# Kernel tuning notes

Hardware: AMD Instinct MI355X
Metric: run time of the kernel (lower is better)

The kernel has to match this reference:

```python
import jax, jax.numpy as jnp
import numpy as np


def _lstm_layer(x_seq, w_ih, w_hh, b_ih, b_hh):
    # x_seq: [T, in], PyTorch gate order i, f, g, o
    H = w_hh.shape[1]
    h0 = jnp.zeros((H,), x_seq.dtype)

    def step(carry, x_t):
        h, c = carry
        gates = x_t @ w_ih.T + h @ w_hh.T + b_ih + b_hh  # [4H]
        i, f, g, o = jnp.split(gates, 4)
        i = jax.nn.sigmoid(i)
        f = jax.nn.sigmoid(f)
        g = jnp.tanh(g)
        o = jax.nn.sigmoid(o)
        c = f * c + i * g
        h = o * jnp.tanh(c)
        return (h, c), h

    _, hs = jax.lax.scan(step, (h0, h0), x_seq)
    return hs  # [T, H]


def setup_inputs() -> dict:
    key = jax.random.key(0)
    ks = jax.random.split(key, 12)
    B, T, n, H = 8, 128, 32, 128
    s = 1.0 / np.sqrt(H)

    def u(k, shape):
        return jax.random.uniform(k, shape, jnp.float32, -s, s)

    return {
        "x": jax.random.normal(ks[0], (B, T, n, n), jnp.float32),
        "w_ih0": u(ks[1], (4 * H, 1)),
        "w_hh0": u(ks[2], (4 * H, H)),
        "b_ih0": u(ks[3], (4 * H,)),
        "b_hh0": u(ks[4], (4 * H,)),
        "w_ih1": u(ks[5], (4 * H, H)),
        "w_hh1": u(ks[6], (4 * H, H)),
        "b_ih1": u(ks[7], (4 * H,)),
        "b_hh1": u(ks[8], (4 * H,)),
        "w_out": u(ks[9], (1, H)),
        "b_out": u(ks[10], (1,)),
    }


def reference(x, w_ih0, w_hh0, b_ih0, b_hh0, w_ih1, w_hh1, b_ih1, b_hh1, w_out, b_out):
    # x: [B, T, n, n]
    def rnn_forward(xi):  # xi: [T, n, n] -> out [T, 1]
        u = jnp.trace(xi, axis1=-2, axis2=-1)[:, None]  # [T, 1]
        h1 = _lstm_layer(u, w_ih0, w_hh0, b_ih0, b_hh0)
        h2 = _lstm_layer(h1, w_ih1, w_hh1, b_ih1, b_hh1)
        return h2 @ w_out.T + b_out  # [T, 1]

    jac = jax.vmap(jax.jacrev(rnn_forward))(x)  # [B, T, 1, T, n, n]
    d = jnp.diagonal(jac, axis1=1, axis2=3)      # [B, 1, n, n, T]
    # mirror torch: [:, 0] then transpose(2,3).transpose(1,2) -> [B, T, n, n]
    return jnp.transpose(d[:, 0], (0, 3, 1, 2))
```

## Files before the change

kernel.cpp:

```cpp
#include <hip/hip_runtime.h>
#include <math.h>

#define H    128
#define TT   128
#define CH   8
#define NCH  (TT / CH)

#define OFF_H1V   0
#define OFF_PARTS 262144
#define OFF_CNT   1441792

__device__ __forceinline__ float sigf(float x)       { return 1.0f / (1.0f + __expf(-x)); }
__device__ __forceinline__ float tanhf_fast(float x) { return 1.0f - 2.0f / (1.0f + __expf(2.0f * x)); }

__device__ __forceinline__ float quad_sum(float v) {
    int t = __builtin_amdgcn_update_dpp(0, __float_as_int(v), 0xB1, 0xF, 0xF, true);
    v += __int_as_float(t);
    t = __builtin_amdgcn_update_dpp(0, __float_as_int(v), 0x4E, 0xF, 0xF, true);
    v += __int_as_float(t);
    return v;
}

__device__ __forceinline__ void wait_ge(int* ptr, int val) {
    while (__hip_atomic_load(ptr, __ATOMIC_RELAXED, __HIP_MEMORY_SCOPE_AGENT) < val)
        __builtin_amdgcn_s_sleep(1);
    (void)__hip_atomic_load(ptr, __ATOMIC_ACQUIRE, __HIP_MEMORY_SCOPE_AGENT);
}

#define BARRIER_LGKM() do { \
    asm volatile("s_waitcnt lgkmcnt(0)" ::: "memory"); \
    __builtin_amdgcn_s_barrier(); \
    asm volatile("" ::: "memory"); \
} while (0)

#define BARRIER_ALL() do { \
    asm volatile("s_waitcnt vmcnt(0) lgkmcnt(0)" ::: "memory"); \
    __builtin_amdgcn_s_barrier(); \
    asm volatile("" ::: "memory"); \
} while (0)

#define DECLW4(nm, src) \
    float4 _t_##nm = (src); \
    float nm##_x = _t_##nm.x, nm##_y = _t_##nm.y, nm##_z = _t_##nm.z, nm##_w = _t_##nm.w; \
    asm volatile("" : "+v"(nm##_x), "+v"(nm##_y), "+v"(nm##_z), "+v"(nm##_w));

#define LOADW_ALL(W) \
    const float4* wpa_ = (const float4*)((W) + (size_t)(rg)       * H + p * 32); \
    const float4* wpb_ = (const float4*)((W) + (size_t)(rg + 128) * H + p * 32); \
    const float4* wpc_ = (const float4*)((W) + (size_t)(rg + 256) * H + p * 32); \
    const float4* wpd_ = (const float4*)((W) + (size_t)(rg + 384) * H + p * 32); \
    DECLW4(wa0, wpa_[0]) DECLW4(wa1, wpa_[1]) DECLW4(wa2, wpa_[2]) DECLW4(wa3, wpa_[3]) \
    DECLW4(wa4, wpa_[4]) DECLW4(wa5, wpa_[5]) DECLW4(wa6, wpa_[6]) DECLW4(wa7, wpa_[7]) \
    DECLW4(wb0, wpb_[0]) DECLW4(wb1, wpb_[1]) DECLW4(wb2, wpb_[2]) DECLW4(wb3, wpb_[3]) \
    DECLW4(wb4, wpb_[4]) DECLW4(wb5, wpb_[5]) DECLW4(wb6, wpb_[6]) DECLW4(wb7, wpb_[7]) \
    DECLW4(wc0, wpc_[0]) DECLW4(wc1, wpc_[1]) DECLW4(wc2, wpc_[2]) DECLW4(wc3, wpc_[3]) \
    DECLW4(wc4, wpc_[4]) DECLW4(wc5, wpc_[5]) DECLW4(wc6, wpc_[6]) DECLW4(wc7, wpc_[7]) \
    DECLW4(wd0, wpd_[0]) DECLW4(wd1, wpd_[1]) DECLW4(wd2, wpd_[2]) DECLW4(wd3, wpd_[3]) \
    DECLW4(wd4, wpd_[4]) DECLW4(wd5, wpd_[5]) DECLW4(wd6, wpd_[6]) DECLW4(wd7, wpd_[7])

#define FMA1(nm, ov, acc) \
    acc = fmaf(nm##_x, ov.x, acc); acc = fmaf(nm##_y, ov.y, acc); \
    acc = fmaf(nm##_z, ov.z, acc); acc = fmaf(nm##_w, ov.w, acc);

#define DOTJ(j) FMA1(wa##j, hv##j, a0) FMA1(wb##j, hv##j, a1) FMA1(wc##j, hv##j, a2) FMA1(wd##j, hv##j, a3)

#define DOT_BODY(HBASE) \
    const float4* _hp4 = (const float4*)(HBASE); \
    float4 hv0=_hp4[0],hv1=_hp4[1],hv2=_hp4[2],hv3=_hp4[3], \
           hv4=_hp4[4],hv5=_hp4[5],hv6=_hp4[6],hv7=_hp4[7]; \
    float a0=0.f,a1=0.f,a2=0.f,a3=0.f; \
    DOTJ(0) DOTJ(1) DOTJ(2) DOTJ(3) DOTJ(4) DOTJ(5) DOTJ(6) DOTJ(7) \
    a0 = quad_sum(a0); a1 = quad_sum(a1); a2 = quad_sum(a2); a3 = quad_sum(a3);

__global__ __launch_bounds__(512, 1)
void pipe_kernel(const float* __restrict__ x,
                 const float* __restrict__ w_ih0,
                 const float* __restrict__ w_hh0,
                 const float* __restrict__ b_ih0,
                 const float* __restrict__ b_hh0,
                 const float* __restrict__ w_ih1,
                 const float* __restrict__ w_hh1,
                 const float* __restrict__ b_ih1,
                 const float* __restrict__ b_hh1,
                 const float* __restrict__ w_out,
                 float* __restrict__ ws,
                 float* __restrict__ outp) {
    const int role = blockIdx.x >> 3;
    const int b    = blockIdx.x & 7;
    const int r    = threadIdx.x;
    const int rg   = r >> 2, p = r & 3;
    const int wsl  = rg >> 5, wpos = rg & 31;

    int* cntA  = (int*)ws + OFF_CNT       + b * 32;
    int* cntB1 = (int*)ws + OFF_CNT + 256 + b * 32;
    int* cntB2 = (int*)ws + OFF_CNT + 512 + b * 32;
    float* h1v = ws + OFF_H1V + (size_t)b * TT * 256;

    __shared__ float hbuf[2][144];
    __shared__ float u_s[TT];
    __shared__ float scr[512];
    __shared__ float hb[CH * 144];
    __shared__ float gbuf[CH][128];

    if (role == 0) {
        LOADW_ALL(w_hh0)
        const float b0 = b_ih0[rg]       + b_hh0[rg];
        const float b1 = b_ih0[rg + 128] + b_hh0[rg + 128];
        const float b2 = b_ih0[rg + 256] + b_hh0[rg + 256];
        const float b3 = b_ih0[rg + 384] + b_hh0[rg + 384];
        const float wi0 = w_ih0[rg], wi1 = w_ih0[rg + 128];
        const float wi2 = w_ih0[rg + 256], wi3 = w_ih0[rg + 384];
        {
            const float* xb = x + (size_t)(b * TT + (r & 127)) * 1024;
            const int pq = r >> 7;
            float u = 0.f;
#pragma unroll
            for (int i = 0; i < 8; i++) u += xb[(pq * 8 + i) * 33];
            scr[r] = u;
        }
        if (r < 144) hbuf[0][r] = 0.f;
        __syncthreads();
        if (r < TT) u_s[r] = scr[r] + scr[r + 128] + scr[r + 256] + scr[r + 384];
        __syncthreads();

        float c1 = 0.f;
        float hn_prev = 0.f, vn_prev = 0.f;
        for (int t = 0; t < TT; t++) {
            if (t & (CH - 1)) {
                if (p == 0) h1v[(t - 1) * 256 + rg] = hn_prev;
                if (p == 1) h1v[(t - 1) * 256 + 128 + rg] = vn_prev;
            }
            const float u = u_s[t];
            const float* hc = hbuf[t & 1];
            float* hx = hbuf[(t & 1) ^ 1];
            DOT_BODY(hc + p * 36)
            float z0 = a0 + fmaf(wi0, u, b0);
            float z1 = a1 + fmaf(wi1, u, b1);
            float z2 = a2 + fmaf(wi2, u, b2);
            float z3 = a3 + fmaf(wi3, u, b3);
            float gi = sigf(z0), gf = sigf(z1), gg = tanhf_fast(z2), go = sigf(z3);
            float di = gi * (1.f - gi) * wi0, df = gf * (1.f - gf) * wi1;
            float dg = (1.f - gg * gg) * wi2, dd = go * (1.f - go) * wi3;
            float dc = df * c1 + di * gg + gi * dg;
            c1 = gf * c1 + gi * gg;
            float th = tanhf_fast(c1);
            float hn = go * th;
            float vn = dd * th + go * (1.f - th * th) * dc;
            if (p == wsl) hx[p * 36 + wpos] = hn;
            if ((t & (CH - 1)) == CH - 1) {
                if (p == 0) h1v[t * 256 + rg] = hn;
                if (p == 1) h1v[t * 256 + 128 + rg] = vn;
                BARRIER_ALL();
                if (r == 0)
                    __hip_atomic_store(cntA, t + 1, __ATOMIC_RELEASE, __HIP_MEMORY_SCOPE_AGENT);
            } else {
                hn_prev = hn; vn_prev = vn;
                BARRIER_LGKM();
            }
        }
    } else if (role == 1 || role == 2) {
        LOADW_ALL(w_ih1)
        int* myCnt = (role == 2) ? cntB2 : cntB1;
        const float* hsrc = h1v + ((role == 2) ? 128 : 0);
        float* pbase = ws + OFF_PARTS + (size_t)b * TT * 1024 + ((role == 2) ? 512 : 0);
        for (int c = 0; c < NCH; c++) {
            if (r == 0) wait_ge(cntA, (c + 1) * CH);
            __syncthreads();
            if (r < 256) {
                int tl = r >> 5, k4 = r & 31, s = k4 >> 3, j = k4 & 7;
                float4 v = *(const float4*)(hsrc + (size_t)(c * CH + tl) * 256 + k4 * 4);
                *(float4*)&hb[(tl * 4 + s) * 36 + j * 4] = v;
            }
            __syncthreads();
#pragma unroll
            for (int tl = 0; tl < CH; tl++) {
                DOT_BODY(hb + (tl * 4 + p) * 36)
                float sel = (p == 0) ? a0 : (p == 1) ? a1 : (p == 2) ? a2 : a3;
                pbase[(size_t)(c * CH + tl) * 1024 + r] = sel;
            }
            BARRIER_ALL();
            if (r == 0)
                __hip_atomic_store(myCnt, (c + 1) * CH, __ATOMIC_RELEASE, __HIP_MEMORY_SCOPE_AGENT);
        }
    } else {
        LOADW_ALL(w_hh1)
        const float b0 = b_ih1[rg]       + b_hh1[rg];
        const float b1 = b_ih1[rg + 128] + b_hh1[rg + 128];
        const float b2 = b_ih1[rg + 256] + b_hh1[rg + 256];
        const float b3 = b_ih1[rg + 384] + b_hh1[rg + 384];
        const float wo = w_out[rg];
        if (r < 144) hbuf[0][r] = 0.f;
        __syncthreads();
        const float* parts = ws + OFF_PARTS + (size_t)b * TT * 1024;
        float c2 = 0.f;
        for (int c = 0; c < NCH; c++) {
            if (r == 0) { wait_ge(cntB1, (c + 1) * CH); wait_ge(cntB2, (c + 1) * CH); }
            __syncthreads();
            float4 zf[CH], af[CH];
#pragma unroll
            for (int tl = 0; tl < CH; tl++) {
                zf[tl] = *(const float4*)(parts + (size_t)(c * CH + tl) * 1024 + rg * 4);
                af[tl] = *(const float4*)(parts + (size_t)(c * CH + tl) * 1024 + 512 + rg * 4);
            }
#pragma unroll
            for (int tl = 0; tl < CH; tl++) {
                const int t = c * CH + tl;
                const float* hc = hbuf[t & 1];
                float* hx = hbuf[(t & 1) ^ 1];
                DOT_BODY(hc + p * 36)
                float z0 = a0 + b0 + zf[tl].x;
                float z1 = a1 + b1 + zf[tl].y;
                float z2 = a2 + b2 + zf[tl].z;
                float z3 = a3 + b3 + zf[tl].w;
                float gi = sigf(z0), gf = sigf(z1), gg = tanhf_fast(z2), go = sigf(z3);
                float di = gi * (1.f - gi) * af[tl].x, df = gf * (1.f - gf) * af[tl].y;
                float dg = (1.f - gg * gg) * af[tl].z, dd = go * (1.f - go) * af[tl].w;
                float dc = df * c2 + di * gg + gi * dg;
                c2 = gf * c2 + gi * gg;
                float th = tanhf_fast(c2);
                if (p == wsl) hx[p * 36 + wpos] = go * th;
                float dh2 = dd * th + go * (1.f - th * th) * dc;
                if (p == 0) gbuf[tl][rg] = wo * dh2;
                BARRIER_LGKM();
            }
            {
                const int w = r >> 6, l = r & 63;
                float v = gbuf[w][l] + gbuf[w][l + 64];
                v = quad_sum(v);
                v += __shfl_xor(v, 4, 64);
                v += __shfl_xor(v, 8, 64);
                v += __shfl_xor(v, 16, 64);
                v += __shfl_xor(v, 32, 64);
                if (l == 0) scr[w] = v;
                BARRIER_LGKM();
                if (r < 256) {
                    const int tl = r >> 5, d = r & 31;
                    outp[(size_t)(b * TT + c * CH + tl) * 1024 + d * 33] = scr[tl];
                }
            }
        }
    }
}

extern "C" void kernel_launch(void* const* d_in, const int* in_sizes, int n_in,
                              void* d_out, int out_size, void* d_ws, size_t ws_size,
                              hipStream_t stream) {
    const float* x     = (const float*)d_in[0];
    const float* w_ih0 = (const float*)d_in[1];
    const float* w_hh0 = (const float*)d_in[2];
    const float* b_ih0 = (const float*)d_in[3];
    const float* b_hh0 = (const float*)d_in[4];
    const float* w_ih1 = (const float*)d_in[5];
    const float* w_hh1 = (const float*)d_in[6];
    const float* b_ih1 = (const float*)d_in[7];
    const float* b_hh1 = (const float*)d_in[8];
    const float* w_out = (const float*)d_in[9];

    float* ws = (float*)d_ws;

    hipMemsetAsync(d_out, 0, (size_t)out_size, stream);

    pipe_kernel<<<dim3(32), dim3(512), 0, stream>>>(x, w_ih0, w_hh0, b_ih0, b_hh0,
                                                    w_ih1, w_hh1, b_ih1, b_hh1, w_out,
                                                    ws, (float*)d_out);
}
```

Measured before the change: 240.3 us.

## Split LSTM recurrent dot products across 8 lanes with 1024-thread blocks

Doubles the block size to 1024 threads so each gate row's 128-wide dot product is split across 8 lanes of 16 elements instead of 4 lanes of 32. The extra cross-lane step uses a DPP row reduction, and the shared hidden-state buffers are re-laid out with a stride of 20. The aim is to shorten the serial per-timestep critical path of the recurrence and halve the per-thread weight registers. In exchange, barriers now span twice as many waves, reductions gain a step, and the layer-2 block loads its pre-activations per step instead of prefetching a whole chunk.

```diff
diff --git a/kernel.cpp b/kernel.cpp
--- a/kernel.cpp
+++ b/kernel.cpp
@@ -20,6 +20,11 @@
     v += __int_as_float(t);
     return v;
 }
+__device__ __forceinline__ float sum8(float v) {
+    v = quad_sum(v);
+    int t = __builtin_amdgcn_update_dpp(0, __float_as_int(v), 0x141, 0xF, 0xF, true);
+    return v + __int_as_float(t);
+}
 
 __device__ __forceinline__ void wait_ge(int* ptr, int val) {
     while (__hip_atomic_load(ptr, __ATOMIC_RELAXED, __HIP_MEMORY_SCOPE_AGENT) < val)
@@ -45,18 +50,14 @@
     asm volatile("" : "+v"(nm##_x), "+v"(nm##_y), "+v"(nm##_z), "+v"(nm##_w));
 
 #define LOADW_ALL(W) \
-    const float4* wpa_ = (const float4*)((W) + (size_t)(rg)       * H + p * 32); \
-    const float4* wpb_ = (const float4*)((W) + (size_t)(rg + 128) * H + p * 32); \
-    const float4* wpc_ = (const float4*)((W) + (size_t)(rg + 256) * H + p * 32); \
-    const float4* wpd_ = (const float4*)((W) + (size_t)(rg + 384) * H + p * 32); \
+    const float4* wpa_ = (const float4*)((W) + (size_t)(rg)       * H + p * 16); \
+    const float4* wpb_ = (const float4*)((W) + (size_t)(rg + 128) * H + p * 16); \
+    const float4* wpc_ = (const float4*)((W) + (size_t)(rg + 256) * H + p * 16); \
+    const float4* wpd_ = (const float4*)((W) + (size_t)(rg + 384) * H + p * 16); \
     DECLW4(wa0, wpa_[0]) DECLW4(wa1, wpa_[1]) DECLW4(wa2, wpa_[2]) DECLW4(wa3, wpa_[3]) \
-    DECLW4(wa4, wpa_[4]) DECLW4(wa5, wpa_[5]) DECLW4(wa6, wpa_[6]) DECLW4(wa7, wpa_[7]) \
     DECLW4(wb0, wpb_[0]) DECLW4(wb1, wpb_[1]) DECLW4(wb2, wpb_[2]) DECLW4(wb3, wpb_[3]) \
-    DECLW4(wb4, wpb_[4]) DECLW4(wb5, wpb_[5]) DECLW4(wb6, wpb_[6]) DECLW4(wb7, wpb_[7]) \
     DECLW4(wc0, wpc_[0]) DECLW4(wc1, wpc_[1]) DECLW4(wc2, wpc_[2]) DECLW4(wc3, wpc_[3]) \
-    DECLW4(wc4, wpc_[4]) DECLW4(wc5, wpc_[5]) DECLW4(wc6, wpc_[6]) DECLW4(wc7, wpc_[7]) \
-    DECLW4(wd0, wpd_[0]) DECLW4(wd1, wpd_[1]) DECLW4(wd2, wpd_[2]) DECLW4(wd3, wpd_[3]) \
-    DECLW4(wd4, wpd_[4]) DECLW4(wd5, wpd_[5]) DECLW4(wd6, wpd_[6]) DECLW4(wd7, wpd_[7])
+    DECLW4(wd0, wpd_[0]) DECLW4(wd1, wpd_[1]) DECLW4(wd2, wpd_[2]) DECLW4(wd3, wpd_[3])
 
 #define FMA1(nm, ov, acc) \
     acc = fmaf(nm##_x, ov.x, acc); acc = fmaf(nm##_y, ov.y, acc); \
@@ -66,13 +67,15 @@
 
 #define DOT_BODY(HBASE) \
     const float4* _hp4 = (const float4*)(HBASE); \
-    float4 hv0=_hp4[0],hv1=_hp4[1],hv2=_hp4[2],hv3=_hp4[3], \
-           hv4=_hp4[4],hv5=_hp4[5],hv6=_hp4[6],hv7=_hp4[7]; \
+    float4 hv0=_hp4[0],hv1=_hp4[1],hv2=_hp4[2],hv3=_hp4[3]; \
     float a0=0.f,a1=0.f,a2=0.f,a3=0.f; \
-    DOTJ(0) DOTJ(1) DOTJ(2) DOTJ(3) DOTJ(4) DOTJ(5) DOTJ(6) DOTJ(7) \
-    a0 = quad_sum(a0); a1 = quad_sum(a1); a2 = quad_sum(a2); a3 = quad_sum(a3);
-
-__global__ __launch_bounds__(512, 1)
+    DOTJ(0) DOTJ(1) DOTJ(2) DOTJ(3) \
+    a0 = sum8(a0); a1 = sum8(a1); a2 = sum8(a2); a3 = sum8(a3);
+
+#define SLS 20
+#define HSZ (8 * SLS)
+
+__global__ __launch_bounds__(1024, 1)
 void pipe_kernel(const float* __restrict__ x,
                  const float* __restrict__ w_ih0,
                  const float* __restrict__ w_hh0,
@@ -88,18 +91,18 @@
     const int role = blockIdx.x >> 3;
     const int b    = blockIdx.x & 7;
     const int r    = threadIdx.x;
-    const int rg   = r >> 2, p = r & 3;
-    const int wsl  = rg >> 5, wpos = rg & 31;
+    const int rg   = r >> 3, p = r & 7;
+    const int wsl  = rg >> 4, wpos = rg & 15;
 
     int* cntA  = (int*)ws + OFF_CNT       + b * 32;
     int* cntB1 = (int*)ws + OFF_CNT + 256 + b * 32;
     int* cntB2 = (int*)ws + OFF_CNT + 512 + b * 32;
     float* h1v = ws + OFF_H1V + (size_t)b * TT * 256;
 
-    __shared__ float hbuf[2][144];
+    __shared__ float hbuf[2][HSZ];
     __shared__ float u_s[TT];
-    __shared__ float scr[512];
-    __shared__ float hb[CH * 144];
+    __shared__ float scr[1024];
+    __shared__ float hb[CH * HSZ];
     __shared__ float gbuf[CH][128];
 
     if (role == 0) {
@@ -115,12 +118,17 @@
             const int pq = r >> 7;
             float u = 0.f;
 #pragma unroll
-            for (int i = 0; i < 8; i++) u += xb[(pq * 8 + i) * 33];
+            for (int i = 0; i < 4; i++) u += xb[(pq * 4 + i) * 33];
             scr[r] = u;
         }
-        if (r < 144) hbuf[0][r] = 0.f;
+        if (r < HSZ) hbuf[0][r] = 0.f;
         __syncthreads();
-        if (r < TT) u_s[r] = scr[r] + scr[r + 128] + scr[r + 256] + scr[r + 384];
+        if (r < TT) {
+            float s = 0.f;
+#pragma unroll
+            for (int k = 0; k < 8; k++) s += scr[r + 128 * k];
+            u_s[r] = s;
+        }
         __syncthreads();
 
         float c1 = 0.f;
@@ -133,7 +141,7 @@
             const float u = u_s[t];
             const float* hc = hbuf[t & 1];
             float* hx = hbuf[(t & 1) ^ 1];
-            DOT_BODY(hc + p * 36)
+            DOT_BODY(hc + p * SLS)
             float z0 = a0 + fmaf(wi0, u, b0);
             float z1 = a1 + fmaf(wi1, u, b1);
             float z2 = a2 + fmaf(wi2, u, b2);
@@ -146,7 +154,7 @@
             float th = tanhf_fast(c1);
             float hn = go * th;
             float vn = dd * th + go * (1.f - th * th) * dc;
-            if (p == wsl) hx[p * 36 + wpos] = hn;
+            if (p == wsl) hx[p * SLS + wpos] = hn;
             if ((t & (CH - 1)) == CH - 1) {
                 if (p == 0) h1v[t * 256 + rg] = hn;
                 if (p == 1) h1v[t * 256 + 128 + rg] = vn;
@@ -167,16 +175,18 @@
             if (r == 0) wait_ge(cntA, (c + 1) * CH);
             __syncthreads();
             if (r < 256) {
-                int tl = r >> 5, k4 = r & 31, s = k4 >> 3, j = k4 & 7;
+                int tl = r >> 5, k4 = r & 31;
                 float4 v = *(const float4*)(hsrc + (size_t)(c * CH + tl) * 256 + k4 * 4);
-                *(float4*)&hb[(tl * 4 + s) * 36 + j * 4] = v;
+                *(float4*)&hb[tl * HSZ + (k4 >> 2) * SLS + (k4 & 3) * 4] = v;
             }
             __syncthreads();
 #pragma unroll
             for (int tl = 0; tl < CH; tl++) {
-                DOT_BODY(hb + (tl * 4 + p) * 36)
-                float sel = (p == 0) ? a0 : (p == 1) ? a1 : (p == 2) ? a2 : a3;
-                pbase[(size_t)(c * CH + tl) * 1024 + r] = sel;
+                DOT_BODY(hb + tl * HSZ + p * SLS)
+                if (p < 4) {
+                    float sel = (p == 0) ? a0 : (p == 1) ? a1 : (p == 2) ? a2 : a3;
+                    pbase[(size_t)(c * CH + tl) * 1024 + rg * 4 + p] = sel;
+                }
             }
             BARRIER_ALL();
             if (r == 0)
@@ -189,49 +199,48 @@
         const float b2 = b_ih1[rg + 256] + b_hh1[rg + 256];
         const float b3 = b_ih1[rg + 384] + b_hh1[rg + 384];
         const float wo = w_out[rg];
-        if (r < 144) hbuf[0][r] = 0.f;
+        if (r < HSZ) hbuf[0][r] = 0.f;
         __syncthreads();
         const float* parts = ws + OFF_PARTS + (size_t)b * TT * 1024;
         float c2 = 0.f;
         for (int c = 0; c < NCH; c++) {
             if (r == 0) { wait_ge(cntB1, (c + 1) * CH); wait_ge(cntB2, (c + 1) * CH); }
             __syncthreads();
-            float4 zf[CH], af[CH];
-#pragma unroll
-            for (int tl = 0; tl < CH; tl++) {
-                zf[tl] = *(const float4*)(parts + (size_t)(c * CH + tl) * 1024 + rg * 4);
-                af[tl] = *(const float4*)(parts + (size_t)(c * CH + tl) * 1024 + 512 + rg * 4);
-            }
 #pragma unroll
             for (int tl = 0; tl < CH; tl++) {
                 const int t = c * CH + tl;
+                const float* pt = parts + (size_t)t * 1024 + rg * 4;
+                float4 zf = *(const float4*)pt;
+                float4 af = *(const float4*)(pt + 512);
                 const float* hc = hbuf[t & 1];
                 float* hx = hbuf[(t & 1) ^ 1];
-                DOT_BODY(hc + p * 36)
-                float z0 = a0 + b0 + zf[tl].x;
-                float z1 = a1 + b1 + zf[tl].y;
-                float z2 = a2 + b2 + zf[tl].z;
-                float z3 = a3 + b3 + zf[tl].w;
+                DOT_BODY(hc + p * SLS)
+                float z0 = a0 + b0 + zf.x;
+                float z1 = a1 + b1 + zf.y;
+                float z2 = a2 + b2 + zf.z;
+                float z3 = a3 + b3 + zf.w;
                 float gi = sigf(z0), gf = sigf(z1), gg = tanhf_fast(z2), go = sigf(z3);
-                float di = gi * (1.f - gi) * af[tl].x, df = gf * (1.f - gf) * af[tl].y;
-                float dg = (1.f - gg * gg) * af[tl].z, dd = go * (1.f - go) * af[tl].w;
+                float di = gi * (1.f - gi) * af.x, df = gf * (1.f - gf) * af.y;
+                float dg = (1.f - gg * gg) * af.z, dd = go * (1.f - go) * af.w;
                 float dc = df * c2 + di * gg + gi * dg;
                 c2 = gf * c2 + gi * gg;
                 float th = tanhf_fast(c2);
-                if (p == wsl) hx[p * 36 + wpos] = go * th;
+                if (p == wsl) hx[p * SLS + wpos] = go * th;
                 float dh2 = dd * th + go * (1.f - th * th) * dc;
                 if (p == 0) gbuf[tl][rg] = wo * dh2;
                 BARRIER_LGKM();
             }
             {
-                const int w = r >> 6, l = r & 63;
-                float v = gbuf[w][l] + gbuf[w][l + 64];
-                v = quad_sum(v);
-                v += __shfl_xor(v, 4, 64);
-                v += __shfl_xor(v, 8, 64);
-                v += __shfl_xor(v, 16, 64);
-                v += __shfl_xor(v, 32, 64);
-                if (l == 0) scr[w] = v;
+                if (r < 512) {
+                    const int w = r >> 6, l = r & 63;
+                    float v = gbuf[w][l] + gbuf[w][l + 64];
+                    v = quad_sum(v);
+                    v += __shfl_xor(v, 4, 64);
+                    v += __shfl_xor(v, 8, 64);
+                    v += __shfl_xor(v, 16, 64);
+                    v += __shfl_xor(v, 32, 64);
+                    if (l == 0) scr[w] = v;
+                }
                 BARRIER_LGKM();
                 if (r < 256) {
                     const int tl = r >> 5, d = r & 31;
@@ -260,7 +269,7 @@
 
     hipMemsetAsync(d_out, 0, (size_t)out_size, stream);
 
-    pipe_kernel<<<dim3(32), dim3(512), 0, stream>>>(x, w_ih0, w_hh0, b_ih0, b_hh0,
-                                                    w_ih1, w_hh1, b_ih1, b_hh1, w_out,
-                                                    ws, (float*)d_out);
-}
+    pipe_kernel<<<dim3(32), dim3(1024), 0, stream>>>(x, w_ih0, w_hh0, b_ih0, b_hh0,
+                                                     w_ih1, w_hh1, b_ih1, b_hh1, w_out,
+                                                     ws, (float*)d_out);
+}
```

Result: slower. 285.5 us (+18.8%).

## Remap thread layout and broadcast h via DPP to cut LDS reads

Applied to the files above, without the earlier changes.

Threads are remapped so each lane loads only two float4 of the hidden state from LDS instead of eight. The remaining values are broadcast across each group of four lanes with DPP quad permutes, and the cross-slice reduction uses row-shift DPP sums. The consumer role now loads its per-step partials inside the loop instead of prefetching a whole chunk into registers, and the launch bounds loosen to allow up to two waves per EU. The aim is to lower LDS bandwidth and latency on the serial recurrent critical path, at the cost of extra DPP instructions and possibly more exposed global-load latency.

```diff
diff --git a/kernel.cpp b/kernel.cpp
--- a/kernel.cpp
+++ b/kernel.cpp
@@ -13,6 +13,13 @@
 __device__ __forceinline__ float sigf(float x)       { return 1.0f / (1.0f + __expf(-x)); }
 __device__ __forceinline__ float tanhf_fast(float x) { return 1.0f - 2.0f / (1.0f + __expf(2.0f * x)); }
 
+__device__ __forceinline__ float sum4s(float v) {
+    int t = __builtin_amdgcn_update_dpp(0, __float_as_int(v), 0x124, 0xF, 0xF, true);
+    v += __int_as_float(t);
+    t = __builtin_amdgcn_update_dpp(0, __float_as_int(v), 0x128, 0xF, 0xF, true);
+    v += __int_as_float(t);
+    return v;
+}
 __device__ __forceinline__ float quad_sum(float v) {
     int t = __builtin_amdgcn_update_dpp(0, __float_as_int(v), 0xB1, 0xF, 0xF, true);
     v += __int_as_float(t);
@@ -58,21 +65,30 @@
     DECLW4(wd0, wpd_[0]) DECLW4(wd1, wpd_[1]) DECLW4(wd2, wpd_[2]) DECLW4(wd3, wpd_[3]) \
     DECLW4(wd4, wpd_[4]) DECLW4(wd5, wpd_[5]) DECLW4(wd6, wpd_[6]) DECLW4(wd7, wpd_[7])
 
-#define FMA1(nm, ov, acc) \
-    acc = fmaf(nm##_x, ov.x, acc); acc = fmaf(nm##_y, ov.y, acc); \
-    acc = fmaf(nm##_z, ov.z, acc); acc = fmaf(nm##_w, ov.w, acc);
-
-#define DOTJ(j) FMA1(wa##j, hv##j, a0) FMA1(wb##j, hv##j, a1) FMA1(wc##j, hv##j, a2) FMA1(wd##j, hv##j, a3)
-
-#define DOT_BODY(HBASE) \
-    const float4* _hp4 = (const float4*)(HBASE); \
-    float4 hv0=_hp4[0],hv1=_hp4[1],hv2=_hp4[2],hv3=_hp4[3], \
-           hv4=_hp4[4],hv5=_hp4[5],hv6=_hp4[6],hv7=_hp4[7]; \
-    float a0=0.f,a1=0.f,a2=0.f,a3=0.f; \
-    DOTJ(0) DOTJ(1) DOTJ(2) DOTJ(3) DOTJ(4) DOTJ(5) DOTJ(6) DOTJ(7) \
-    a0 = quad_sum(a0); a1 = quad_sum(a1); a2 = quad_sum(a2); a3 = quad_sum(a3);
-
-__global__ __launch_bounds__(512, 1)
+#define QB(dst, src, ctrl) \
+    dst = __int_as_float(__builtin_amdgcn_update_dpp(0, __float_as_int(src), ctrl, 0xF, 0xF, true));
+
+#define FMAQ(g, A, B, acc) \
+    acc = fmaf(g##A##_x, h0_, acc); acc = fmaf(g##A##_y, h1_, acc); \
+    acc = fmaf(g##A##_z, h2_, acc); acc = fmaf(g##A##_w, h3_, acc); \
+    acc = fmaf(g##B##_x, h4_, acc); acc = fmaf(g##B##_y, h5_, acc); \
+    acc = fmaf(g##B##_z, h6_, acc); acc = fmaf(g##B##_w, h7_, acc);
+
+#define QUARTER(A, B, ctrl) { \
+    float h0_, h1_, h2_, h3_, h4_, h5_, h6_, h7_; \
+    QB(h0_, hA_.x, ctrl) QB(h1_, hA_.y, ctrl) QB(h2_, hA_.z, ctrl) QB(h3_, hA_.w, ctrl) \
+    QB(h4_, hB_.x, ctrl) QB(h5_, hB_.y, ctrl) QB(h6_, hB_.z, ctrl) QB(h7_, hB_.w, ctrl) \
+    FMAQ(wa, A, B, a0) FMAQ(wb, A, B, a1) FMAQ(wc, A, B, a2) FMAQ(wd, A, B, a3) }
+
+#define DOT_BODY(HB) \
+    const float4* _hq = (const float4*)((HB) + p * 36 + lo * 8); \
+    float4 hA_ = _hq[0], hB_ = _hq[1]; \
+    float a0 = 0.f, a1 = 0.f, a2 = 0.f, a3 = 0.f; \
+    QUARTER(0, 1, 0x00) QUARTER(2, 3, 0x55) QUARTER(4, 5, 0xAA) QUARTER(6, 7, 0xFF) \
+    a0 = sum4s(a0); a1 = sum4s(a1); a2 = sum4s(a2); a3 = sum4s(a3);
+
+__global__ __launch_bounds__(512)
+__attribute__((amdgpu_waves_per_eu(1, 2)))
 void pipe_kernel(const float* __restrict__ x,
                  const float* __restrict__ w_ih0,
                  const float* __restrict__ w_hh0,
@@ -88,7 +104,9 @@
     const int role = blockIdx.x >> 3;
     const int b    = blockIdx.x & 7;
     const int r    = threadIdx.x;
-    const int rg   = r >> 2, p = r & 3;
+    const int p    = (r >> 2) & 3;
+    const int lo   = r & 3;
+    const int rg   = lo | ((r >> 4) << 2);
     const int wsl  = rg >> 5, wpos = rg & 31;
 
     int* cntA  = (int*)ws + OFF_CNT       + b * 32;
@@ -96,10 +114,10 @@
     int* cntB2 = (int*)ws + OFF_CNT + 512 + b * 32;
     float* h1v = ws + OFF_H1V + (size_t)b * TT * 256;
 
-    __shared__ float hbuf[2][144];
+    __shared__ __align__(16) float hbuf[2][144];
     __shared__ float u_s[TT];
     __shared__ float scr[512];
-    __shared__ float hb[CH * 144];
+    __shared__ __align__(16) float hb[CH * 144];
     __shared__ float gbuf[CH][128];
 
     if (role == 0) {
@@ -133,7 +151,7 @@
             const float u = u_s[t];
             const float* hc = hbuf[t & 1];
             float* hx = hbuf[(t & 1) ^ 1];
-            DOT_BODY(hc + p * 36)
+            DOT_BODY(hc)
             float z0 = a0 + fmaf(wi0, u, b0);
             float z1 = a1 + fmaf(wi1, u, b1);
             float z2 = a2 + fmaf(wi2, u, b2);
@@ -146,7 +164,7 @@
             float th = tanhf_fast(c1);
             float hn = go * th;
             float vn = dd * th + go * (1.f - th * th) * dc;
-            if (p == wsl) hx[p * 36 + wpos] = hn;
+            if (p == wsl) hx[wsl * 36 + wpos] = hn;
             if ((t & (CH - 1)) == CH - 1) {
                 if (p == 0) h1v[t * 256 + rg] = hn;
                 if (p == 1) h1v[t * 256 + 128 + rg] = vn;
@@ -163,6 +181,7 @@
         int* myCnt = (role == 2) ? cntB2 : cntB1;
         const float* hsrc = h1v + ((role == 2) ? 128 : 0);
         float* pbase = ws + OFF_PARTS + (size_t)b * TT * 1024 + ((role == 2) ? 512 : 0);
+        const int sidx = (rg << 2) | p;
         for (int c = 0; c < NCH; c++) {
             if (r == 0) wait_ge(cntA, (c + 1) * CH);
             __syncthreads();
@@ -174,9 +193,9 @@
             __syncthreads();
 #pragma unroll
             for (int tl = 0; tl < CH; tl++) {
-                DOT_BODY(hb + (tl * 4 + p) * 36)
+                DOT_BODY(hb + tl * 144)
                 float sel = (p == 0) ? a0 : (p == 1) ? a1 : (p == 2) ? a2 : a3;
-                pbase[(size_t)(c * CH + tl) * 1024 + r] = sel;
+                pbase[(size_t)(c * CH + tl) * 1024 + sidx] = sel;
             }
             BARRIER_ALL();
             if (r == 0)
@@ -196,29 +215,26 @@
         for (int c = 0; c < NCH; c++) {
             if (r == 0) { wait_ge(cntB1, (c + 1) * CH); wait_ge(cntB2, (c + 1) * CH); }
             __syncthreads();
-            float4 zf[CH], af[CH];
-#pragma unroll
-            for (int tl = 0; tl < CH; tl++) {
-                zf[tl] = *(const float4*)(parts + (size_t)(c * CH + tl) * 1024 + rg * 4);
-                af[tl] = *(const float4*)(parts + (size_t)(c * CH + tl) * 1024 + 512 + rg * 4);
-            }
 #pragma unroll
             for (int tl = 0; tl < CH; tl++) {
                 const int t = c * CH + tl;
+                const float* pt = parts + (size_t)t * 1024 + rg * 4;
+                float4 zf = *(const float4*)pt;
+                float4 af = *(const float4*)(pt + 512);
                 const float* hc = hbuf[t & 1];
                 float* hx = hbuf[(t & 1) ^ 1];
-                DOT_BODY(hc + p * 36)
-                float z0 = a0 + b0 + zf[tl].x;
-                float z1 = a1 + b1 + zf[tl].y;
-                float z2 = a2 + b2 + zf[tl].z;
-                float z3 = a3 + b3 + zf[tl].w;
+                DOT_BODY(hc)
+                float z0 = a0 + b0 + zf.x;
+                float z1 = a1 + b1 + zf.y;
+                float z2 = a2 + b2 + zf.z;
+                float z3 = a3 + b3 + zf.w;
                 float gi = sigf(z0), gf = sigf(z1), gg = tanhf_fast(z2), go = sigf(z3);
-                float di = gi * (1.f - gi) * af[tl].x, df = gf * (1.f - gf) * af[tl].y;
-                float dg = (1.f - gg * gg) * af[tl].z, dd = go * (1.f - go) * af[tl].w;
+                float di = gi * (1.f - gi) * af.x, df = gf * (1.f - gf) * af.y;
+                float dg = (1.f - gg * gg) * af.z, dd = go * (1.f - go) * af.w;
                 float dc = df * c2 + di * gg + gi * dg;
                 c2 = gf * c2 + gi * gg;
                 float th = tanhf_fast(c2);
-                if (p == wsl) hx[p * 36 + wpos] = go * th;
+                if (p == wsl) hx[wsl * 36 + wpos] = go * th;
                 float dh2 = dd * th + go * (1.f - th * th) * dc;
                 if (p == 0) gbuf[tl][rg] = wo * dh2;
                 BARRIER_LGKM();
```

Measured after the change: 277.4 us. +15.5%, slower.
